# Kernel tuning notes

Measured on AMD Instinct MI355X. Metric: run time of the kernel, lower is better.

The kernel has to match this reference:

```python
import jax, jax.numpy as jnp
import numpy as np

NH = 8    # num_heads
HD = 64   # head_dim
EPS = 1e-6


def setup_inputs() -> dict:
    key = jax.random.key(0)
    ks = jax.random.split(key, 8)
    B, N, D = 16, 3136, 512
    x = jax.random.normal(ks[0], (B, N, D), jnp.float32)
    Wq = jax.random.normal(ks[1], (D, D), jnp.float32) * 0.02
    Wkv = jax.random.normal(ks[2], (D, 2 * D), jnp.float32) * 0.02
    pos_enc = jax.random.normal(ks[3], (1, N, D), jnp.float32) * 0.02
    # depthwise conv: fan_out = k*k*out/groups = 25
    dwc_w = jax.random.normal(ks[4], (HD, 1, 5, 5), jnp.float32) * np.sqrt(2.0 / 25.0).astype(np.float32)
    dwc_b = jnp.zeros((HD,), jnp.float32)
    Wp = jax.random.normal(ks[5], (D, D), jnp.float32) * 0.02
    bp = jnp.zeros((D,), jnp.float32)
    return {"x": x, "Wq": Wq, "Wkv": Wkv, "pos_enc": pos_enc,
            "dwc_w": dwc_w, "dwc_b": dwc_b, "Wp": Wp, "bp": bp,
            "H": 56, "W": 56}


def reference(x, Wq, Wkv, pos_enc, dwc_w, dwc_b, Wp, bp, H, W):
    B, N, D = x.shape
    # projections (qkv_bias=False)
    q = jax.nn.relu(x @ Wq)                       # ReLU feature map on q
    kv = x @ Wkv                                  # [B, N, 2D]
    k = jax.nn.relu(kv[..., :D] + pos_enc)        # pos enc added before ReLU kernel
    v = kv[..., D:]
    # split heads: b n (h c) -> b h n c
    qh = q.reshape(B, N, NH, HD).transpose(0, 2, 1, 3)
    kh = k.reshape(B, N, NH, HD).transpose(0, 2, 1, 3)
    vh = v.reshape(B, N, NH, HD).transpose(0, 2, 1, 3)
    # linear attention: normalization and KV context
    k_sum = kh.sum(axis=2)                                        # [B, NH, HD]
    d_inv = 1.0 / (jnp.einsum('bhnd,bhd->bhn', qh, k_sum) + EPS)  # [B, NH, N]
    ctx = jnp.einsum('bhmd,bhme->bhde', kh, vh)                   # [B, NH, HD, HD]
    attn = jnp.einsum('bhnd,bhde->bhne', qh, ctx) * d_inv[..., None]
    # depthwise conv positional mixing on v (N == H*W)
    fmap = vh.reshape(B * NH, H, W, HD).transpose(0, 3, 1, 2)     # [(b h), c, H, W]
    dwc = jax.lax.conv_general_dilated(
        fmap, dwc_w, window_strides=(1, 1), padding='SAME',
        feature_group_count=HD,
        dimension_numbers=('NCHW', 'OIHW', 'NCHW')) + dwc_b[None, :, None, None]
    dwc = dwc.transpose(0, 2, 3, 1).reshape(B, NH, N, HD)
    # NOTE: original torch code reshapes ((b h), n, c) -> (B, N, D) directly
    # (NOT the inverse rearrange); reproduce that exact flat reshape.
    out = (attn + dwc).reshape(B, N, D)
    return out @ Wp + bp
```

## Files before the change

kernel.cpp:

```cpp
#include <hip/hip_runtime.h>

__device__ __forceinline__ float b2f(ushort u) {
    union { float f; unsigned int i; } w; w.i = ((unsigned int)u) << 16; return w.f;
}
__device__ __forceinline__ ushort f2b(float f) {
    union { float f; unsigned int i; } w; w.f = f;
    unsigned int lsb = (w.i >> 16) & 1u;
    w.i += 0x7fffu + lsb;
    return (ushort)(w.i >> 16);
}

typedef __bf16 bf16x8 __attribute__((ext_vector_type(8)));
typedef float floatx4 __attribute__((ext_vector_type(4)));

__device__ __forceinline__ void async_copy16(ushort* lds_base, const ushort* gptr) {
    __builtin_amdgcn_global_load_lds(
        (const __attribute__((address_space(1))) unsigned int*)gptr,
        (__attribute__((address_space(3))) unsigned int*)lds_base,
        16, 0, 0);
}

#define BATCH 16
#define NTOK  3136
#define NHEAD 8
#define HDIM  64
#define HSP   56
#define MROWS (BATCH * NTOK)
#define KDIM  512

__global__ __launch_bounds__(256) void detect_dtype(const ushort* __restrict__ x,
                                                    int* __restrict__ flag)
{
    __shared__ int s;
    if (threadIdx.x == 0) s = 0;
    __syncthreads();
    int bad = 0;
    for (int i = threadIdx.x; i < 4096; i += 256) {
        int e = (x[i] >> 7) & 0xFF;
        if (e >= 0x90) bad = 1;
    }
    if (bad) s = 1;
    __syncthreads();
    if (threadIdx.x == 0) flag[0] = s;
}

__global__ __launch_bounds__(256) void convert_x(
    const void* __restrict__ x, const int* __restrict__ flag,
    ushort* __restrict__ xbf)
{
    size_t t = (size_t)blockIdx.x * 256 + threadIdx.x;
    if (flag[0]) {
        const float* xf = (const float*)x + t * 8;
        float4 f0 = *(const float4*)xf;
        float4 f1 = *(const float4*)(xf + 4);
        ushort o[8] = { f2b(f0.x), f2b(f0.y), f2b(f0.z), f2b(f0.w),
                        f2b(f1.x), f2b(f1.y), f2b(f1.z), f2b(f1.w) };
        *(uint4*)(xbf + t * 8) = *(const uint4*)o;
    } else {
        *(uint4*)(xbf + t * 8) = *((const uint4*)x + t);
    }
}

__global__ __launch_bounds__(256) void prep_weights(
    const void* __restrict__ Wq, const void* __restrict__ Wkv,
    const void* __restrict__ Wp, const int* __restrict__ flag,
    ushort* __restrict__ WqkvT, ushort* __restrict__ WpT)
{
    bool f32 = flag[0] != 0;
    int idx = blockIdx.x * 256 + threadIdx.x;
    int kk = idx & 511;
    int n  = idx >> 9;
    if (n < 1536) {
        ushort val;
        if (n < 512)
            val = f32 ? f2b(((const float*)Wq)[kk * 512 + n])
                      : ((const ushort*)Wq)[kk * 512 + n];
        else
            val = f32 ? f2b(((const float*)Wkv)[kk * 1024 + (n - 512)])
                      : ((const ushort*)Wkv)[kk * 1024 + (n - 512)];
        WqkvT[n * 512 + kk] = val;
    } else {
        int n2 = n - 1536;
        WpT[n2 * 512 + kk] = f32 ? f2b(((const float*)Wp)[kk * 512 + n2])
                                 : ((const ushort*)Wp)[kk * 512 + n2];
    }
}

__global__ __launch_bounds__(256) void prep_dwc(
    const void* __restrict__ dwc_w, const void* __restrict__ dwc_b,
    const int* __restrict__ flag, float* __restrict__ wT)
{
    bool f32 = flag[0] != 0;
    for (int i = threadIdx.x; i < 1600; i += 256) {
        int e = i / 25, tap = i % 25;
        float w = f32 ? ((const float*)dwc_w)[i] : b2f(((const ushort*)dwc_w)[i]);
        wT[tap * 64 + e] = w;
    }
    if (threadIdx.x < 64) {
        float b = f32 ? ((const float*)dwc_b)[threadIdx.x]
                      : b2f(((const ushort*)dwc_b)[threadIdx.x]);
        wT[1600 + threadIdx.x] = b;
    }
}

__device__ __forceinline__ int swz(int r) { return (r ^ (r >> 2)) & 3; }

#define VMWAIT(N) asm volatile("s_waitcnt vmcnt(" #N ")" ::: "memory")
#define LGKM0()   do { asm volatile("s_waitcnt lgkmcnt(0)" ::: "memory"); \
                       __builtin_amdgcn_sched_barrier(0); } while (0)
#define ASLOT(u) (((u) % 3) * 4096)
#define BSLOT(u) (12288 + ((u) % 3) * 8192)

__global__ __launch_bounds__(256, 2) void gemm256_bt(
    const ushort* __restrict__ A, const ushort* __restrict__ Bt,
    int mode, const int* __restrict__ flag,
    const void* __restrict__ pos_enc, const void* __restrict__ bias,
    void* __restrict__ out0, ushort* __restrict__ out1, ushort* __restrict__ out2,
    int ntn)
{
    __shared__ ushort smem[36864];

    const bool f32 = flag[0] != 0;
    const int tid = threadIdx.x;
    const int lam = tid & 63;
    const int w   = tid >> 6;
    const int wm  = w >> 1;
    const int wn  = w & 1;
    const int g    = lam >> 4;
    const int mrow = lam & 15;

    const int nwg = gridDim.x;
    const int q8  = nwg >> 3;
    const int bid = blockIdx.x;
    const int fid = (bid & 7) * q8 + (bid >> 3);
    const int tm = fid / ntn, tn = fid - tm * ntn;
    const int m0 = tm * 128, n0 = tn * 256;

    const int scol8 = 8 * ((lam & 3) ^ ((lam >> 3) & 3));
    const int srowA = w * 32 + (lam >> 2);
    const int srowB = w * 64 + (lam >> 2);
    const ushort* gA = A  + (size_t)(m0 + srowA) * KDIM + scol8;
    const ushort* gB = Bt + (size_t)(n0 + srowB) * KDIM + scol8;

    const int axor  = (g ^ ((mrow >> 1) & 3)) << 3;
    const int aBase = (wm * 64 + mrow) * 32 + axor;
    const int bBase = (wn * 128 + mrow) * 32 + axor;

    floatx4 acc[4][8];
    #pragma unroll
    for (int i = 0; i < 4; i++)
        #pragma unroll
        for (int j = 0; j < 8; j++) acc[i][j] = (floatx4)0.f;

#define STGA(u) do { \
    async_copy16(smem + ASLOT(u) + w * 1024,       gA + (u) * 32); \
    async_copy16(smem + ASLOT(u) + w * 1024 + 512, gA + 16 * KDIM + (u) * 32); } while (0)
#define STGB(u) do { \
    async_copy16(smem + BSLOT(u) + w * 2048,        gB + (u) * 32); \
    async_copy16(smem + BSLOT(u) + w * 2048 + 512,  gB + 16 * KDIM + (u) * 32); \
    async_copy16(smem + BSLOT(u) + w * 2048 + 1024, gB + 32 * KDIM + (u) * 32); \
    async_copy16(smem + BSLOT(u) + w * 2048 + 1536, gB + 48 * KDIM + (u) * 32); } while (0)

    STGA(0); STGB(0);
    STGA(1); STGB(1);
    VMWAIT(6);
    __builtin_amdgcn_s_barrier();

    #pragma unroll
    for (int u = 0; u < 16; ++u) {
        if (u <= 13) { STGA(u + 2); STGB(u + 2); }

        const ushort* sa = smem + ASLOT(u) + aBase;
        const ushort* sb = smem + BSLOT(u) + bBase;
        bf16x8 a[4], bfr[8];
        #pragma unroll
        for (int fr = 0; fr < 4; ++fr) a[fr] = *(const bf16x8*)(sa + fr * 512);
        #pragma unroll
        for (int fc = 0; fc < 8; ++fc) bfr[fc] = *(const bf16x8*)(sb + fc * 512);
        LGKM0();

        __builtin_amdgcn_s_setprio(1);
        #pragma unroll
        for (int fr = 0; fr < 4; ++fr)
            #pragma unroll
            for (int fc = 0; fc < 8; ++fc)
                acc[fr][fc] = __builtin_amdgcn_mfma_f32_16x16x32_bf16(
                    bfr[fc], a[fr], acc[fr][fc], 0, 0, 0);
        __builtin_amdgcn_s_setprio(0);

        if (u <= 13)      VMWAIT(6);
        else if (u == 14) VMWAIT(0);
        if (u < 15) __builtin_amdgcn_s_barrier();
    }

    const int cb0 = n0 + wn * 128;
    const int tz  = cb0 >> 9;
    #pragma unroll
    for (int fr = 0; fr < 4; ++fr) {
        const int rg  = m0 + wm * 64 + fr * 16 + mrow;
        const int bb2 = rg / NTOK;
        const int nn  = rg - bb2 * NTOK;
        if (mode == 1) {
            if (f32) {
                float* orow = (float*)out0 + (size_t)rg * 512 + cb0 + g * 4;
                #pragma unroll
                for (int fc = 0; fc < 8; ++fc) {
                    float ob[4];
                    #pragma unroll
                    for (int r = 0; r < 4; ++r)
                        ob[r] = acc[fr][fc][r] +
                                ((const float*)bias)[cb0 + fc * 16 + g * 4 + r];
                    *(float4*)(orow + fc * 16) = *(const float4*)ob;
                }
            } else {
                ushort* orow = (ushort*)out0 + (size_t)rg * 512 + cb0 + g * 4;
                #pragma unroll
                for (int fc = 0; fc < 8; ++fc) {
                    ushort t4[4];
                    #pragma unroll
                    for (int r = 0; r < 4; ++r)
                        t4[r] = f2b(acc[fr][fc][r] +
                                    b2f(((const ushort*)bias)[cb0 + fc * 16 + g * 4 + r]));
                    *(uint2*)(orow + fc * 16) = *(const uint2*)t4;
                }
            }
        } else {
            #pragma unroll
            for (int fc = 0; fc < 8; ++fc) {
                const int colg = cb0 + fc * 16 + g * 4;
                const int head = (colg >> 6) & 7;
                const size_t obase =
                    (((size_t)bb2 * 8 + head) * NTOK + nn) * 64 + (colg & 63);
                ushort t4[4];
                if (tz == 0) {
                    #pragma unroll
                    for (int r = 0; r < 4; ++r)
                        t4[r] = f2b(fmaxf(acc[fr][fc][r], 0.f));
                    *(uint2*)((ushort*)out0 + obase) = *(const uint2*)t4;
                } else if (tz == 1) {
                    const int d0 = colg - 512;
                    #pragma unroll
                    for (int r = 0; r < 4; ++r) {
                        float pe = f32
                            ? ((const float*)pos_enc)[(size_t)nn * 512 + d0 + r]
                            : b2f(((const ushort*)pos_enc)[(size_t)nn * 512 + d0 + r]);
                        t4[r] = f2b(fmaxf(acc[fr][fc][r] + pe, 0.f));
                    }
                    *(uint2*)(out1 + obase) = *(const uint2*)t4;
                } else {
                    #pragma unroll
                    for (int r = 0; r < 4; ++r)
                        t4[r] = f2b(acc[fr][fc][r]);
                    *(uint2*)(out2 + obase) = *(const uint2*)t4;
                }
            }
        }
    }
#undef STGA
#undef STGB
}

#define SPLITS 7
#define NPER   (NTOK / SPLITS)

__global__ __launch_bounds__(256) void ctx_ksum(
    const ushort* __restrict__ kbuf, const ushort* __restrict__ vbuf,
    float* __restrict__ ctx, float* __restrict__ ksum)
{
    __shared__ ushort kT[64 * 32];
    __shared__ ushort vT[64 * 32];
    __shared__ float ks4[256];
    int bh = blockIdx.x, sp = blockIdx.y;
    int tid = threadIdx.x;
    int lane = tid & 63, wave = tid >> 6;
    int mrow = lane & 15, g = lane >> 4;
    int r = tid & 31, cblk = tid >> 5;
    size_t base = ((size_t)bh * NTOK + sp * NPER) * 64;

    floatx4 acc[4];
    #pragma unroll
    for (int c = 0; c < 4; c++) acc[c] = (floatx4)0.f;
    float kpart = 0.f;
    int kd = tid >> 2, kq = tid & 3;

    for (int nc = 0; nc < NPER; nc += 32) {
        uint4 ku = *(const uint4*)(kbuf + base + (size_t)(nc + r) * 64 + cblk * 8);
        uint4 vu = *(const uint4*)(vbuf + base + (size_t)(nc + r) * 64 + cblk * 8);
        __syncthreads();
        const ushort* kp = (const ushort*)&ku;
        const ushort* vp = (const ushort*)&vu;
        #pragma unroll
        for (int j = 0; j < 8; j++) {
            int d = cblk * 8 + j;
            int blk = (r >> 3) ^ swz(d);
            kT[d * 32 + blk * 8 + (r & 7)] = kp[j];
            vT[d * 32 + blk * 8 + (r & 7)] = vp[j];
        }
        __syncthreads();
        {
            const ushort* p = &kT[kd * 32 + kq * 8];
            #pragma unroll
            for (int j = 0; j < 8; j++) kpart += b2f(p[j]);
        }
        int dr = wave * 16 + mrow;
        bf16x8 af = *(const bf16x8*)&kT[dr * 32 + (g ^ swz(dr)) * 8];
        #pragma unroll
        for (int c = 0; c < 4; c++) {
            int er = c * 16 + mrow;
            bf16x8 bf = *(const bf16x8*)&vT[er * 32 + (g ^ swz(er)) * 8];
            acc[c] = __builtin_amdgcn_mfma_f32_16x16x32_bf16(af, bf, acc[c], 0, 0, 0);
        }
    }
    #pragma unroll
    for (int c = 0; c < 4; c++)
        #pragma unroll
        for (int rr = 0; rr < 4; rr++) {
            int d = wave * 16 + g * 4 + rr;
            int e = c * 16 + mrow;
            atomicAdd(&ctx[bh * 4096 + d * 64 + e], acc[c][rr]);
        }
    ks4[tid] = kpart;
    __syncthreads();
    if (tid < 64) {
        float s = ks4[tid * 4] + ks4[tid * 4 + 1] + ks4[tid * 4 + 2] + ks4[tid * 4 + 3];
        atomicAdd(&ksum[bh * 64 + tid], s);
    }
}

__global__ __launch_bounds__(256) void attn_kernel(
    const ushort* __restrict__ q, const float* __restrict__ ctx,
    const float* __restrict__ ksum, ushort* __restrict__ ybuf)
{
    __shared__ float smem[4352];
    ushort* ctxT = (ushort*)smem;
    float* sout = smem;
    int bh = blockIdx.x, cg = blockIdx.y;
    int tid = threadIdx.x;
    int lane = tid & 63, wave = tid >> 6;
    int mrow = lane & 15, g = lane >> 4;

    for (int i = tid; i < 640; i += 256) {
        int e = i >> 3, blk = i & 7;
        ushort tmp[8];
        #pragma unroll
        for (int j = 0; j < 8; j++) {
            int d = blk * 8 + j;
            float v = 0.f;
            if (e < 64) v = ctx[bh * 4096 + d * 64 + e];
            else if (e == 64) v = ksum[bh * 64 + d];
            tmp[j] = f2b(v);
        }
        *(uint4*)&ctxT[e * 64 + (blk ^ (e & 7)) * 8] = *(const uint4*)tmp;
    }
    __syncthreads();

    bf16x8 bfr[2][5];
    #pragma unroll
    for (int kt = 0; kt < 2; kt++)
        #pragma unroll
        for (int c = 0; c < 5; c++) {
            int e = c * 16 + mrow;
            bfr[kt][c] = *(const bf16x8*)&ctxT[e * 64 + ((kt * 4 + g) ^ (e & 7)) * 8];
        }

    int token4 = tid >> 2, seg = tid & 3;
    for (int cc = 0; cc < 7; cc++) {
        int n0 = (cg * 7 + cc) * 64;
        floatx4 acc[5];
        #pragma unroll
        for (int c = 0; c < 5; c++) acc[c] = (floatx4)0.f;
        size_t qrow = ((size_t)bh * NTOK + n0 + wave * 16 + mrow) * 64;
        #pragma unroll
        for (int kt = 0; kt < 2; kt++) {
            bf16x8 af = *(const bf16x8*)(q + qrow + kt * 32 + g * 8);
            #pragma unroll
            for (int c = 0; c < 5; c++)
                acc[c] = __builtin_amdgcn_mfma_f32_16x16x32_bf16(af, bfr[kt][c], acc[c], 0, 0, 0);
        }
        __syncthreads();
        #pragma unroll
        for (int c = 0; c < 4; c++)
            #pragma unroll
            for (int rr = 0; rr < 4; rr++)
                sout[(wave * 16 + g * 4 + rr) * 68 + c * 16 + mrow] = acc[c][rr];
        if (mrow == 0) {
            #pragma unroll
            for (int rr = 0; rr < 4; rr++)
                sout[(wave * 16 + g * 4 + rr) * 68 + 64] = acc[4][rr];
        }
        __syncthreads();
        float dinv = 1.0f / (sout[token4 * 68 + 64] + 1e-6f);
        const float* sp = &sout[token4 * 68 + seg * 16];
        ushort res[16];
        #pragma unroll
        for (int j = 0; j < 16; j++) res[j] = f2b(sp[j] * dinv);
        ushort* o = ybuf + ((size_t)bh * NTOK + n0 + token4) * 64 + seg * 16;
        *(uint4*)o = *(const uint4*)res;
        *(uint4*)(o + 8) = *(const uint4*)(res + 8);
    }
}

__global__ __launch_bounds__(256) void dwc_add(
    const ushort* __restrict__ v, const float* __restrict__ wT,
    ushort* __restrict__ ybuf)
{
    __shared__ float wls[1664];
    for (int i = threadIdx.x; i < 1664; i += 256) wls[i] = wT[i];
    __syncthreads();

    int t = blockIdx.x * 256 + threadIdx.x;
    int eg = (t & 7) * 8;
    int r = t >> 3;
    int n  = r % NTOK;
    int bh = r / NTOK;
    int y = n / HSP, x = n % HSP;

    float acc[8];
    #pragma unroll
    for (int j = 0; j < 8; j++) acc[j] = wls[1600 + eg + j];

    const ushort* vb = v + (size_t)bh * NTOK * 64 + eg;
    #pragma unroll
    for (int dy = 0; dy < 5; ++dy) {
        int yy = y + dy - 2;
        if (yy < 0 || yy >= HSP) continue;
        #pragma unroll
        for (int dx = 0; dx < 5; ++dx) {
            int xx = x + dx - 2;
            if (xx < 0 || xx >= HSP) continue;
            uint4 u = *(const uint4*)(vb + (size_t)(yy * HSP + xx) * 64);
            const ushort* up = (const ushort*)&u;
            const float* wp = &wls[(dy * 5 + dx) * 64 + eg];
            #pragma unroll
            for (int j = 0; j < 8; j++) acc[j] += wp[j] * b2f(up[j]);
        }
    }
    size_t o = (size_t)r * 64 + eg;
    uint4 yo = *(const uint4*)(ybuf + o);
    const ushort* yp = (const ushort*)&yo;
    ushort res[8];
    #pragma unroll
    for (int j = 0; j < 8; j++) res[j] = f2b(acc[j] + b2f(yp[j]));
    *(uint4*)(ybuf + o) = *(const uint4*)res;
}

extern "C" void kernel_launch(void* const* d_in, const int* in_sizes, int n_in,
                              void* d_out, int out_size, void* d_ws, size_t ws_size,
                              hipStream_t stream) {
    const void* x    = d_in[0];
    const void* Wq   = d_in[1];
    const void* Wkv  = d_in[2];
    const void* pos  = d_in[3];
    const void* dwcw = d_in[4];
    const void* dwcb = d_in[5];
    const void* Wp   = d_in[6];
    const void* bp   = d_in[7];

    char* ws = (char*)d_ws;
    const size_t SZ_BIG = 51380224;
    int*    flag   = (int*)(ws + 0);
    ushort* WqkvT  = (ushort*)(ws + 4096);
    ushort* WpT    = (ushort*)(ws + 4096 + 1572864);
    float*  wTdwc  = (float*)(ws + 2101248);
    float*  ctx    = (float*)(ws + 2107904);
    float*  ksum   = (float*)(ws + 4205056);
    ushort* qbuf   = (ushort*)(ws + 4237824);
    ushort* kbuf   = (ushort*)(ws + 4237824 + SZ_BIG);
    ushort* vbuf   = (ushort*)(ws + 4237824 + 2 * SZ_BIG);
    ushort* xbf = (ushort*)d_out;

    detect_dtype<<<1, 256, 0, stream>>>((const ushort*)x, flag);
    hipMemsetAsync(ctx, 0, 2097152 + 32768, stream);

    prep_weights<<<4096, 256, 0, stream>>>(Wq, Wkv, Wp, flag, WqkvT, WpT);
    prep_dwc<<<1, 256, 0, stream>>>(dwcw, dwcb, flag, wTdwc);
    convert_x<<<12544, 256, 0, stream>>>(x, flag, xbf);

    gemm256_bt<<<dim3(392 * 6), 256, 0, stream>>>(
        xbf, WqkvT, 0, flag, pos, nullptr, qbuf, kbuf, vbuf, 6);

    ctx_ksum<<<dim3(128, SPLITS), 256, 0, stream>>>(kbuf, vbuf, ctx, ksum);

    attn_kernel<<<dim3(128, 7), 256, 0, stream>>>(qbuf, ctx, ksum, kbuf);

    dwc_add<<<12544, 256, 0, stream>>>(vbuf, wTdwc, kbuf);

    gemm256_bt<<<dim3(392 * 2), 256, 0, stream>>>(
        kbuf, WpT, 1, flag, nullptr, bp, d_out, nullptr, nullptr, 2);
}
```

Baseline: 546.3 us.

## Tile depthwise conv through LDS with halo and double ctx_ksum token chunk

The depthwise 5x5 conv now runs one block per (head-batch, 8-channel group, 28x28 quadrant). Each block stages a 32x32 haloed tile of v in LDS and computes all outputs from it, instead of each thread issuing 25 scattered global loads. Separately, ctx_ksum processes 64 tokens per iteration with padded LDS rows and two MFMAs per step, which halves the number of barrier rounds. The cost is extra LDS use per block, a reduced block count for dwc, and redundant halo loads at tile edges.

```diff
diff --git a/kernel.cpp b/kernel.cpp
--- a/kernel.cpp
+++ b/kernel.cpp
@@ -267,8 +267,8 @@
     const ushort* __restrict__ kbuf, const ushort* __restrict__ vbuf,
     float* __restrict__ ctx, float* __restrict__ ksum)
 {
-    __shared__ ushort kT[64 * 32];
-    __shared__ ushort vT[64 * 32];
+    __shared__ ushort kT[64 * 72];
+    __shared__ ushort vT[64 * 72];
     __shared__ float ks4[256];
     int bh = blockIdx.x, sp = blockIdx.y;
     int tid = threadIdx.x;
@@ -283,32 +283,46 @@
     float kpart = 0.f;
     int kd = tid >> 2, kq = tid & 3;
 
-    for (int nc = 0; nc < NPER; nc += 32) {
-        uint4 ku = *(const uint4*)(kbuf + base + (size_t)(nc + r) * 64 + cblk * 8);
-        uint4 vu = *(const uint4*)(vbuf + base + (size_t)(nc + r) * 64 + cblk * 8);
+    for (int nc = 0; nc < NPER; nc += 64) {
+        const ushort* kg = kbuf + base + (size_t)(nc + r) * 64 + cblk * 8;
+        const ushort* vg = vbuf + base + (size_t)(nc + r) * 64 + cblk * 8;
+        uint4 ku0 = *(const uint4*)kg;
+        uint4 ku1 = *(const uint4*)(kg + 32 * 64);
+        uint4 vu0 = *(const uint4*)vg;
+        uint4 vu1 = *(const uint4*)(vg + 32 * 64);
         __syncthreads();
-        const ushort* kp = (const ushort*)&ku;
-        const ushort* vp = (const ushort*)&vu;
+        const ushort* kp0 = (const ushort*)&ku0;
+        const ushort* kp1 = (const ushort*)&ku1;
+        const ushort* vp0 = (const ushort*)&vu0;
+        const ushort* vp1 = (const ushort*)&vu1;
         #pragma unroll
         for (int j = 0; j < 8; j++) {
             int d = cblk * 8 + j;
             int blk = (r >> 3) ^ swz(d);
-            kT[d * 32 + blk * 8 + (r & 7)] = kp[j];
-            vT[d * 32 + blk * 8 + (r & 7)] = vp[j];
+            kT[d * 72 + blk * 8 + (r & 7)]       = kp0[j];
+            kT[d * 72 + (blk + 4) * 8 + (r & 7)] = kp1[j];
+            vT[d * 72 + blk * 8 + (r & 7)]       = vp0[j];
+            vT[d * 72 + (blk + 4) * 8 + (r & 7)] = vp1[j];
         }
         __syncthreads();
         {
-            const ushort* p = &kT[kd * 32 + kq * 8];
-            #pragma unroll
-            for (int j = 0; j < 8; j++) kpart += b2f(p[j]);
+            const ushort* p0 = &kT[kd * 72 + kq * 8];
+            const ushort* p1 = &kT[kd * 72 + (kq + 4) * 8];
+            #pragma unroll
+            for (int j = 0; j < 8; j++) kpart += b2f(p0[j]) + b2f(p1[j]);
         }
         int dr = wave * 16 + mrow;
-        bf16x8 af = *(const bf16x8*)&kT[dr * 32 + (g ^ swz(dr)) * 8];
+        int ab = g ^ swz(dr);
+        bf16x8 af0 = *(const bf16x8*)&kT[dr * 72 + ab * 8];
+        bf16x8 af1 = *(const bf16x8*)&kT[dr * 72 + (ab + 4) * 8];
         #pragma unroll
         for (int c = 0; c < 4; c++) {
             int er = c * 16 + mrow;
-            bf16x8 bf = *(const bf16x8*)&vT[er * 32 + (g ^ swz(er)) * 8];
-            acc[c] = __builtin_amdgcn_mfma_f32_16x16x32_bf16(af, bf, acc[c], 0, 0, 0);
+            int eb = g ^ swz(er);
+            bf16x8 bf0 = *(const bf16x8*)&vT[er * 72 + eb * 8];
+            bf16x8 bf1 = *(const bf16x8*)&vT[er * 72 + (eb + 4) * 8];
+            acc[c] = __builtin_amdgcn_mfma_f32_16x16x32_bf16(af0, bf0, acc[c], 0, 0, 0);
+            acc[c] = __builtin_amdgcn_mfma_f32_16x16x32_bf16(af1, bf1, acc[c], 0, 0, 0);
         }
     }
     #pragma unroll
@@ -405,43 +419,51 @@
     ushort* __restrict__ ybuf)
 {
     __shared__ float wls[1664];
-    for (int i = threadIdx.x; i < 1664; i += 256) wls[i] = wT[i];
+    __shared__ ushort vt[32 * 32 * 8];
+    const int tid = threadIdx.x;
+    for (int i = tid; i < 1664; i += 256) wls[i] = wT[i];
+
+    const int bh = blockIdx.x;
+    const int eg = blockIdx.y;
+    const int qd = blockIdx.z;
+    const int qy = (qd >> 1) * 28, qx = (qd & 1) * 28;
+
+    const ushort* vb = v + (size_t)bh * NTOK * 64 + eg * 8;
+
+    for (int i = tid; i < 1024; i += 256) {
+        int r = i >> 5, c = i & 31;
+        int gy = qy + r - 2, gx = qx + c - 2;
+        uint4 val = make_uint4(0u, 0u, 0u, 0u);
+        if (gy >= 0 && gy < HSP && gx >= 0 && gx < HSP)
+            val = *(const uint4*)(vb + (size_t)(gy * HSP + gx) * 64);
+        *(uint4*)&vt[i * 8] = val;
+    }
     __syncthreads();
 
-    int t = blockIdx.x * 256 + threadIdx.x;
-    int eg = (t & 7) * 8;
-    int r = t >> 3;
-    int n  = r % NTOK;
-    int bh = r / NTOK;
-    int y = n / HSP, x = n % HSP;
-
-    float acc[8];
-    #pragma unroll
-    for (int j = 0; j < 8; j++) acc[j] = wls[1600 + eg + j];
-
-    const ushort* vb = v + (size_t)bh * NTOK * 64 + eg;
-    #pragma unroll
-    for (int dy = 0; dy < 5; ++dy) {
-        int yy = y + dy - 2;
-        if (yy < 0 || yy >= HSP) continue;
-        #pragma unroll
-        for (int dx = 0; dx < 5; ++dx) {
-            int xx = x + dx - 2;
-            if (xx < 0 || xx >= HSP) continue;
-            uint4 u = *(const uint4*)(vb + (size_t)(yy * HSP + xx) * 64);
-            const ushort* up = (const ushort*)&u;
-            const float* wp = &wls[(dy * 5 + dx) * 64 + eg];
-            #pragma unroll
-            for (int j = 0; j < 8; j++) acc[j] += wp[j] * b2f(up[j]);
-        }
-    }
-    size_t o = (size_t)r * 64 + eg;
-    uint4 yo = *(const uint4*)(ybuf + o);
-    const ushort* yp = (const ushort*)&yo;
-    ushort res[8];
-    #pragma unroll
-    for (int j = 0; j < 8; j++) res[j] = f2b(acc[j] + b2f(yp[j]));
-    *(uint4*)(ybuf + o) = *(const uint4*)res;
+    for (int o = tid; o < 784; o += 256) {
+        const int oy = o / 28, ox = o % 28;
+        float acc[8];
+        #pragma unroll
+        for (int j = 0; j < 8; j++) acc[j] = wls[1600 + eg * 8 + j];
+        #pragma unroll
+        for (int dy = 0; dy < 5; ++dy)
+            #pragma unroll
+            for (int dx = 0; dx < 5; ++dx) {
+                uint4 u = *(const uint4*)&vt[(((oy + dy) << 5) + ox + dx) * 8];
+                const ushort* up = (const ushort*)&u;
+                const float* wp = &wls[(dy * 5 + dx) * 64 + eg * 8];
+                #pragma unroll
+                for (int j = 0; j < 8; j++) acc[j] += wp[j] * b2f(up[j]);
+            }
+        const int n = (qy + oy) * HSP + (qx + ox);
+        const size_t off = ((size_t)bh * NTOK + n) * 64 + eg * 8;
+        uint4 yo = *(const uint4*)(ybuf + off);
+        const ushort* yp = (const ushort*)&yo;
+        ushort res[8];
+        #pragma unroll
+        for (int j = 0; j < 8; j++) res[j] = f2b(acc[j] + b2f(yp[j]));
+        *(uint4*)(ybuf + off) = *(const uint4*)res;
+    }
 }
 
 extern "C" void kernel_launch(void* const* d_in, const int* in_sizes, int n_in,
@@ -483,7 +505,7 @@
 
     attn_kernel<<<dim3(128, 7), 256, 0, stream>>>(qbuf, ctx, ksum, kbuf);
 
-    dwc_add<<<12544, 256, 0, stream>>>(vbuf, wTdwc, kbuf);
+    dwc_add<<<dim3(128, 8, 4), 256, 0, stream>>>(vbuf, wTdwc, kbuf);
 
     gemm256_bt<<<dim3(392 * 2), 256, 0, stream>>>(
         kbuf, WpT, 1, flag, nullptr, bp, d_out, nullptr, nullptr, 2);
```

Result: slower. 575.7 us (+5.4%).
